# Kernel optimization log

Measured on AMD Instinct MI355X. Metric: run time of the kernel, lower is better.

## Reference

```python
import jax, jax.numpy as jnp
import numpy as np

# ---- static config (matches init_kwargs) ----
N, E = 8192, 262144
IN_CH, MP_CH, HID, K = 128, 512, 256, 10
EPS, DELTA = 1e-3, 0.311
TV_COEFF, BAL_COEFF = 0.785, 0.514


def setup_inputs() -> dict:
    key = jax.random.key(0)
    ks = jax.random.split(key, 16)

    def p(k, shape):
        fan_in = shape[0] if len(shape) > 1 else shape[0]
        return (jax.random.normal(k, shape, jnp.float32) / np.sqrt(fan_in)).astype(jnp.float32)

    return {
        "x": jax.random.normal(ks[0], (N, IN_CH), jnp.float32),
        "edge_index": jax.random.randint(ks[1], (2, E), 0, N, jnp.int32),
        "edge_weight": jax.random.uniform(ks[2], (E,), jnp.float32),
        # GTVConv layer 1 / 2 (Linear weight + bias)
        "W1": p(ks[3], (IN_CH, MP_CH)), "b1": jnp.zeros((MP_CH,), jnp.float32),
        "W2": p(ks[4], (MP_CH, MP_CH)), "b2": jnp.zeros((MP_CH,), jnp.float32),
        # pooling MLP [512 -> 256 -> K], relu, no norm
        "Wm1": p(ks[5], (MP_CH, HID)), "bm1": jnp.zeros((HID,), jnp.float32),
        "Wm2": p(ks[6], (HID, K)), "bm2": jnp.zeros((K,), jnp.float32),
    }


def _gtv_conv(x, src, dst, w, W, b):
    """GTVConv: out = elu( h - delta*(D_G h - Gamma h) + b ),
    gamma_ij = w_ij / max(||h_i - h_j||_1, eps), h = x @ W."""
    h = x @ W                                   # [N, C]
    diff = jnp.sum(jnp.abs(h[src] - h[dst]), axis=-1)   # [E]
    gamma = w / jnp.maximum(diff, EPS)                  # [E]
    deg = jnp.zeros(h.shape[0], h.dtype).at[dst].add(gamma)          # [N]
    agg = jnp.zeros_like(h).at[dst].add(gamma[:, None] * h[src])     # Gamma @ h
    out = h - DELTA * (deg[:, None] * h - agg) + b
    return jax.nn.elu(out)


def reference(x, edge_index, edge_weight, W1, b1, W2, b2, Wm1, bm1, Wm2, bm2):
    src, dst = edge_index[0], edge_index[1]

    h = _gtv_conv(x, src, dst, edge_weight, W1, b1)
    h = _gtv_conv(h, src, dst, edge_weight, W2, b2)

    # pooling MLP -> cluster logits s
    s_logits = jax.nn.relu(h @ Wm1 + bm1) @ Wm2 + bm2   # [N, K]

    # dense adjacency (to_dense_adj: duplicate edges accumulate)
    adj = jnp.zeros((N, N), x.dtype).at[src, dst].add(edge_weight)

    s = jax.nn.softmax(s_logits, axis=-1)

    # total-variation loss: sum_ij a_ij * sum_k |s_ik - s_jk| / (2 * nnz(adj))
    tv = jnp.zeros((), x.dtype)
    for k in range(K):  # small fixed loop over clusters, avoids [N,N,K] tensor
        col = s[:, k]
        tv = tv + jnp.sum(adj * jnp.abs(col[:, None] - col[None, :]))
    n_edges = jax.lax.stop_gradient(jnp.count_nonzero(adj).astype(x.dtype))
    tv = tv / (2.0 * n_edges)

    # asymmetric-norm balance loss (AsymCheegerCut)
    idx = N // K + 1                         # rho-quantile index (static)
    quant = jnp.sort(s, axis=0)[N - idx]     # idx-th largest per cluster, [K]
    t = s - quant[None, :]
    asym = jnp.where(t >= 0, (K - 1) * t, -t)
    denom = float(N * (K - 1))
    bal = (denom - jnp.sum(asym)) / denom

    return s_logits, TV_COEFF * tv, BAL_COEFF * bal
```

## Files before the change

kernel.cpp:

```cpp
#include <hip/hip_runtime.h>

#define N_NODES 8192
#define N_EDGES 262144
#define IN_CH 128
#define MP_CH 512
#define HID 256
#define KCL 10
#define EPS_C 0.001f
#define DELTA_C 0.311f
#define TV_COEFF_C 0.785f
#define BAL_COEFF_C 0.514f
#define RANK1 7373

typedef __bf16 bf16x8 __attribute__((ext_vector_type(8)));
typedef float f32x4 __attribute__((ext_vector_type(4)));
typedef unsigned short ushort8 __attribute__((ext_vector_type(8)));

__device__ __forceinline__ float bf2f(unsigned short h) {
  union { unsigned int u; float f; } c; c.u = ((unsigned int)h) << 16; return c.f;
}
__device__ __forceinline__ unsigned short f2bf(float f) {
  union { float f; unsigned int u; } c; c.f = f;
  unsigned int r = c.u + 0x7fffu + ((c.u >> 16) & 1u);
  return (unsigned short)(r >> 16);
}

__global__ void prep_kernel(const float* __restrict__ x, const float* __restrict__ W1,
                            const float* __restrict__ W2, const float* __restrict__ Wm1,
                            unsigned short* __restrict__ xb, unsigned short* __restrict__ W1bt,
                            unsigned short* __restrict__ W2bt, unsigned short* __restrict__ Wm1bt,
                            const int* __restrict__ dst, int* __restrict__ cnt) {
  int i = blockIdx.x * 256 + threadIdx.x;
  if (i < 1048576) { xb[i] = f2bf(x[i]); return; }
  i -= 1048576;
  if (i < 65536) { int n = i >> 7, k = i & 127; W1bt[i] = f2bf(W1[k * MP_CH + n]); return; }
  i -= 65536;
  if (i < 262144) { int n = i >> 9, k = i & 511; W2bt[i] = f2bf(W2[k * MP_CH + n]); return; }
  i -= 262144;
  if (i < 131072) { int n = i >> 9, k = i & 511; Wm1bt[i] = f2bf(Wm1[k * HID + n]); return; }
  i -= 131072;
  if (i < N_EDGES) atomicAdd(&cnt[dst[i]], 1);
}

__global__ __launch_bounds__(1024) void scan_kernel(const int* __restrict__ cnt,
                                                    int* __restrict__ offs,
                                                    int* __restrict__ cursor) {
  __shared__ int ts[1024];
  int t = threadIdx.x;
  int v[8]; int s = 0;
#pragma unroll
  for (int j = 0; j < 8; ++j) { v[j] = cnt[t * 8 + j]; s += v[j]; }
  ts[t] = s; __syncthreads();
  for (int off = 1; off < 1024; off <<= 1) {
    int add = (t >= off) ? ts[t - off] : 0;
    __syncthreads();
    ts[t] += add;
    __syncthreads();
  }
  int base = ts[t] - s;
#pragma unroll
  for (int j = 0; j < 8; ++j) { offs[t * 8 + j] = base; cursor[t * 8 + j] = base; base += v[j]; }
  if (t == 1023) offs[N_NODES] = ts[1023];
}

__global__ void fill_kernel(const int* __restrict__ src, const int* __restrict__ dst,
                            const float* __restrict__ ew, int* __restrict__ cursor,
                            int2* __restrict__ esw) {
  for (int e = blockIdx.x * blockDim.x + threadIdx.x; e < N_EDGES; e += gridDim.x * blockDim.x) {
    int p = atomicAdd(&cursor[dst[e]], 1);
    esw[p] = make_int2(src[e], __float_as_int(ew[e]));
  }
}

__global__ __launch_bounds__(256) void gemm_bt(
    const unsigned short* __restrict__ A, const unsigned short* __restrict__ BT,
    float* __restrict__ C, unsigned short* __restrict__ Cb,
    const float* __restrict__ bias, int N, int K, int epi) {
  __shared__ unsigned short lA[128 * 32];
  __shared__ unsigned short lB[128 * 32];
  int lane = threadIdx.x & 63;
  int wv = threadIdx.x >> 6;
  int tm = blockIdx.y * 128, tn = blockIdx.x * 128;
  int wm = (wv >> 1) * 64, wn = (wv & 1) * 64;
  int rA = lane & 15, quad = lane >> 4;
  f32x4 acc[4][4];
#pragma unroll
  for (int i = 0; i < 4; ++i)
#pragma unroll
    for (int j = 0; j < 4; ++j) acc[i][j] = (f32x4){0.f, 0.f, 0.f, 0.f};

  int arow = wv * 32 + (lane >> 2);
  int acol = (lane & 3) * 8;

  for (int k0 = 0; k0 < K; k0 += 32) {
#pragma unroll
    for (int c = 0; c < 2; ++c) {
      const unsigned short* ga = A + (size_t)(tm + arow + c * 16) * K + k0 + acol;
      __builtin_amdgcn_global_load_lds(
          (const __attribute__((address_space(1))) unsigned int*)ga,
          (__attribute__((address_space(3))) unsigned int*)(lA + (wv * 32 + c * 16) * 32),
          16, 0, 0);
      const unsigned short* gb = BT + (size_t)(tn + arow + c * 16) * K + k0 + acol;
      __builtin_amdgcn_global_load_lds(
          (const __attribute__((address_space(1))) unsigned int*)gb,
          (__attribute__((address_space(3))) unsigned int*)(lB + (wv * 32 + c * 16) * 32),
          16, 0, 0);
    }
    __syncthreads();
    bf16x8 af[4], bfr[4];
#pragma unroll
    for (int i = 0; i < 4; ++i)
      af[i] = *(const bf16x8*)(lA + (wm + i * 16 + rA) * 32 + quad * 8);
#pragma unroll
    for (int j = 0; j < 4; ++j)
      bfr[j] = *(const bf16x8*)(lB + (wn + j * 16 + rA) * 32 + quad * 8);
#pragma unroll
    for (int i = 0; i < 4; ++i)
#pragma unroll
      for (int j = 0; j < 4; ++j)
        acc[i][j] = __builtin_amdgcn_mfma_f32_16x16x32_bf16(af[i], bfr[j], acc[i][j], 0, 0, 0);
    __syncthreads();
  }

#pragma unroll
  for (int i = 0; i < 4; ++i)
#pragma unroll
    for (int j = 0; j < 4; ++j)
#pragma unroll
      for (int r = 0; r < 4; ++r) {
        int row = tm + wm + i * 16 + quad * 4 + r;
        int col = tn + wn + j * 16 + rA;
        float v = acc[i][j][r];
        size_t idx = (size_t)row * N + col;
        if (epi == 1) { v += bias[col]; v = fmaxf(v, 0.f); C[idx] = v; }
        else { Cb[idx] = f2bf(v); }
      }
}

__global__ __launch_bounds__(256, 8) void gtv_node(
    const unsigned short* __restrict__ hb, const float* __restrict__ bias,
    const int2* __restrict__ esw, const int* __restrict__ offs,
    unsigned short* __restrict__ outb) {
  int lane = threadIdx.x & 63;
  int wv = threadIdx.x >> 6;
  int d = __builtin_amdgcn_readfirstlane(blockIdx.x * 4 + wv);
  ushort8 hdv = ((const ushort8*)(hb + (size_t)d * MP_CH))[lane];
  float hd[8], acc[8];
#pragma unroll
  for (int j = 0; j < 8; ++j) { hd[j] = bf2f(hdv[j]); acc[j] = 0.f; }
  int e0 = offs[d], e1 = offs[d + 1];
  int i = e0;
  for (; i + 1 < e1; i += 2) {
    int2 ma = esw[i], mb = esw[i + 1];
    float wa = __int_as_float(ma.y), wb = __int_as_float(mb.y);
    ushort8 va = ((const ushort8*)(hb + (size_t)ma.x * MP_CH))[lane];
    ushort8 vb = ((const ushort8*)(hb + (size_t)mb.x * MP_CH))[lane];
    float pa = 0.f, pb = 0.f;
#pragma unroll
    for (int j = 0; j < 8; ++j) {
      pa += fabsf(hd[j] - bf2f(va[j]));
      pb += fabsf(hd[j] - bf2f(vb[j]));
    }
#pragma unroll
    for (int m = 1; m < 64; m <<= 1) { pa += __shfl_xor(pa, m, 64); pb += __shfl_xor(pb, m, 64); }
    float ga = wa * __builtin_amdgcn_rcpf(fmaxf(pa, EPS_C));
    float gb = wb * __builtin_amdgcn_rcpf(fmaxf(pb, EPS_C));
#pragma unroll
    for (int j = 0; j < 8; ++j)
      acc[j] += ga * (hd[j] - bf2f(va[j])) + gb * (hd[j] - bf2f(vb[j]));
  }
  if (i < e1) {
    int2 m0 = esw[i];
    float w = __int_as_float(m0.y);
    ushort8 sv = ((const ushort8*)(hb + (size_t)m0.x * MP_CH))[lane];
    float part = 0.f;
#pragma unroll
    for (int j = 0; j < 8; ++j) part += fabsf(hd[j] - bf2f(sv[j]));
#pragma unroll
    for (int m = 1; m < 64; m <<= 1) part += __shfl_xor(part, m, 64);
    float g = w * __builtin_amdgcn_rcpf(fmaxf(part, EPS_C));
#pragma unroll
    for (int j = 0; j < 8; ++j) acc[j] += g * (hd[j] - bf2f(sv[j]));
  }
  const f32x4* br = (const f32x4*)(bias + lane * 8);
  f32x4 b0 = br[0], b1 = br[1];
  unsigned short ov[8];
#pragma unroll
  for (int j = 0; j < 8; ++j) {
    float bv = (j < 4) ? b0[j] : b1[j - 4];
    float o = hd[j] - DELTA_C * acc[j] + bv;
    o = (o > 0.f) ? o : (expf(o) - 1.f);
    ov[j] = f2bf(o);
  }
  *((ushort8*)(outb + (size_t)d * MP_CH) + lane) = *(ushort8*)ov;
}

__global__ __launch_bounds__(256) void gemm_small(
    const float* __restrict__ hm, const float* __restrict__ W,
    const float* __restrict__ b, float* __restrict__ out, float* __restrict__ s) {
  __shared__ float lw[HID * KCL];
  __shared__ float lb[KCL];
  for (int i = threadIdx.x; i < HID * KCL; i += 256) lw[i] = W[i];
  if (threadIdx.x < KCL) lb[threadIdx.x] = b[threadIdx.x];
  __syncthreads();
  int lane = threadIdx.x & 63, wv = threadIdx.x >> 6;
  int row = blockIdx.x * 4 + wv;
  f32x4 hv = *(const f32x4*)(hm + (size_t)row * HID + lane * 4);
  float p[KCL];
#pragma unroll
  for (int n = 0; n < KCL; ++n) {
    int k0 = lane * 4;
    p[n] = hv[0] * lw[(k0 + 0) * KCL + n] + hv[1] * lw[(k0 + 1) * KCL + n] +
           hv[2] * lw[(k0 + 2) * KCL + n] + hv[3] * lw[(k0 + 3) * KCL + n];
  }
#pragma unroll
  for (int n = 0; n < KCL; ++n)
#pragma unroll
    for (int m = 1; m < 64; m <<= 1) p[n] += __shfl_xor(p[n], m, 64);
  if (lane == 0) {
    float vv[KCL]; float mx = -1e30f;
#pragma unroll
    for (int n = 0; n < KCL; ++n) {
      vv[n] = p[n] + lb[n];
      out[(size_t)row * KCL + n] = vv[n];
      mx = fmaxf(mx, vv[n]);
    }
    float sum = 0.f;
#pragma unroll
    for (int n = 0; n < KCL; ++n) { vv[n] = expf(vv[n] - mx); sum += vv[n]; }
    float inv = 1.f / sum;
#pragma unroll
    for (int n = 0; n < KCL; ++n) s[(size_t)row * KCL + n] = vv[n] * inv;
  }
}

__global__ __launch_bounds__(256) void tv_kernel(
    const int* __restrict__ src, const int* __restrict__ dst,
    const float* __restrict__ ew, const float* __restrict__ s,
    unsigned int* __restrict__ bitmap, float* __restrict__ tv_sum) {
  float local = 0.f;
  for (int e = blockIdx.x * blockDim.x + threadIdx.x; e < N_EDGES; e += gridDim.x * blockDim.x) {
    int a = src[e], b = dst[e];
    float w = ew[e];
    const float* sa = s + (size_t)a * KCL;
    const float* sb = s + (size_t)b * KCL;
    float t = 0.f;
#pragma unroll
    for (int k = 0; k < KCL; ++k) t += fabsf(sa[k] - sb[k]);
    local += w * t;
    if (w != 0.f) {
      unsigned int key = ((unsigned int)a << 13) | (unsigned int)b;
      atomicOr(&bitmap[key >> 5], 1u << (key & 31u));
    }
  }
#pragma unroll
  for (int m = 1; m < 64; m <<= 1) local += __shfl_xor(local, m, 64);
  __shared__ float wsum[4];
  int lane = threadIdx.x & 63, wv = threadIdx.x >> 6;
  if (lane == 0) wsum[wv] = local;
  __syncthreads();
  if (threadIdx.x == 0) atomicAdd(tv_sum, wsum[0] + wsum[1] + wsum[2] + wsum[3]);
}

__global__ __launch_bounds__(256) void popc_kernel(const unsigned int* __restrict__ bm,
                                                   int* __restrict__ cnt) {
  int local = 0;
  for (int i = blockIdx.x * blockDim.x + threadIdx.x; i < (1 << 21); i += gridDim.x * blockDim.x)
    local += __popc(bm[i]);
#pragma unroll
  for (int m = 1; m < 64; m <<= 1) local += __shfl_xor(local, m, 64);
  __shared__ int wsum[4];
  int lane = threadIdx.x & 63, wv = threadIdx.x >> 6;
  if (lane == 0) wsum[wv] = local;
  __syncthreads();
  if (threadIdx.x == 0) atomicAdd(cnt, wsum[0] + wsum[1] + wsum[2] + wsum[3]);
}

__global__ __launch_bounds__(1024) void quant_kernel(const float* __restrict__ s,
                                                     float* __restrict__ asym_sum) {
  __shared__ int wcnt[2][16];
  __shared__ float fsum[16];
  int k = blockIdx.x, t = threadIdx.x;
  int lane = t & 63, wv = t >> 6;
  unsigned int v[8];
#pragma unroll
  for (int j = 0; j < 8; ++j)
    v[j] = __float_as_uint(s[(size_t)(t + j * 1024) * KCL + k]);
  unsigned int lo = 0u, hi = 0x3F800000u;
  int p = 0;
  while (lo < hi) {
    unsigned int mid = (lo + hi) >> 1;
    int c = 0;
#pragma unroll
    for (int j = 0; j < 8; ++j) c += (v[j] <= mid) ? 1 : 0;
#pragma unroll
    for (int m = 1; m < 64; m <<= 1) c += __shfl_xor(c, m, 64);
    if (lane == 0) wcnt[p][wv] = c;
    __syncthreads();
    int tot = 0;
#pragma unroll
    for (int i2 = 0; i2 < 16; ++i2) tot += wcnt[p][i2];
    if (tot >= RANK1) hi = mid; else lo = mid + 1;
    p ^= 1;
  }
  float q = __uint_as_float(lo);
  float local = 0.f;
#pragma unroll
  for (int j = 0; j < 8; ++j) {
    float tt = __uint_as_float(v[j]) - q;
    local += (tt >= 0.f) ? 9.f * tt : -tt;
  }
#pragma unroll
  for (int m = 1; m < 64; m <<= 1) local += __shfl_xor(local, m, 64);
  if (lane == 0) fsum[wv] = local;
  __syncthreads();
  if (t == 0) {
    float tot = 0.f;
#pragma unroll
    for (int i2 = 0; i2 < 16; ++i2) tot += fsum[i2];
    atomicAdd(asym_sum, tot);
  }
}

__global__ void finalize_kernel(const float* __restrict__ scal, const int* __restrict__ ne,
                                float* __restrict__ out) {
  if (threadIdx.x == 0) {
    float tv = scal[0], asym = scal[1];
    float nedges = (float)(*ne);
    out[N_NODES * KCL] = TV_COEFF_C * (tv / (2.f * nedges));
    out[N_NODES * KCL + 1] = BAL_COEFF_C * ((73728.f - asym) / 73728.f);
  }
}

#define OFF_BM     ((size_t)0)
#define OFF_HB     ((size_t)16777216)
#define OFF_OUTB   ((size_t)25165824)
#define OFF_HM     ((size_t)33554432)
#define OFF_XB     ((size_t)41943040)
#define OFF_W1BT   ((size_t)44040192)
#define OFF_W2BT   ((size_t)44171264)
#define OFF_WM1BT  ((size_t)44695552)
#define OFF_S      ((size_t)44957696)
#define OFF_CNT    ((size_t)45285376)
#define OFF_OFFS   ((size_t)45318144)
#define OFF_CURSOR ((size_t)45351168)
#define OFF_SCAL   ((size_t)46432512)

extern "C" void kernel_launch(void* const* d_in, const int* in_sizes, int n_in,
                              void* d_out, int out_size, void* d_ws, size_t ws_size,
                              hipStream_t stream) {
  const float* x   = (const float*)d_in[0];
  const int*   ei  = (const int*)d_in[1];
  const float* ew  = (const float*)d_in[2];
  const float* W1  = (const float*)d_in[3];
  const float* b1  = (const float*)d_in[4];
  const float* W2  = (const float*)d_in[5];
  const float* b2  = (const float*)d_in[6];
  const float* Wm1 = (const float*)d_in[7];
  const float* bm1 = (const float*)d_in[8];
  const float* Wm2 = (const float*)d_in[9];
  const float* bm2 = (const float*)d_in[10];
  float* out = (float*)d_out;

  char* ws = (char*)d_ws;
  unsigned int*   bitmap = (unsigned int*)(ws + OFF_BM);
  unsigned short* hb     = (unsigned short*)(ws + OFF_HB);
  unsigned short* outb   = (unsigned short*)(ws + OFF_OUTB);
  float*          hm     = (float*)(ws + OFF_HM);
  int2*           esw    = (int2*)(ws + OFF_HM);
  unsigned short* xb     = (unsigned short*)(ws + OFF_XB);
  unsigned short* W1bt   = (unsigned short*)(ws + OFF_W1BT);
  unsigned short* W2bt   = (unsigned short*)(ws + OFF_W2BT);
  unsigned short* Wm1bt  = (unsigned short*)(ws + OFF_WM1BT);
  float*          s      = (float*)(ws + OFF_S);
  int*            cnt    = (int*)(ws + OFF_CNT);
  int*            offs   = (int*)(ws + OFF_OFFS);
  int*            cursor = (int*)(ws + OFF_CURSOR);
  float*          scal   = (float*)(ws + OFF_SCAL);
  int*            nep    = (int*)(scal + 2);

  const int* srcA = ei;
  const int* dstA = ei + N_EDGES;

  hipMemsetAsync(cnt, 0, N_NODES * sizeof(int), stream);
  hipMemsetAsync(scal, 0, 64, stream);
  hipMemsetAsync(bitmap, 0, (size_t)1 << 23, stream);

  prep_kernel<<<6912, 256, 0, stream>>>(x, W1, W2, Wm1, xb, W1bt, W2bt, Wm1bt, dstA, cnt);
  scan_kernel<<<1, 1024, 0, stream>>>(cnt, offs, cursor);
  fill_kernel<<<1024, 256, 0, stream>>>(srcA, dstA, ew, cursor, esw);

  gemm_bt<<<dim3(MP_CH / 128, N_NODES / 128), 256, 0, stream>>>(
      xb, W1bt, nullptr, hb, nullptr, MP_CH, IN_CH, 2);
  gtv_node<<<N_NODES / 4, 256, 0, stream>>>(hb, b1, esw, offs, outb);
  gemm_bt<<<dim3(MP_CH / 128, N_NODES / 128), 256, 0, stream>>>(
      outb, W2bt, nullptr, hb, nullptr, MP_CH, MP_CH, 2);
  gtv_node<<<N_NODES / 4, 256, 0, stream>>>(hb, b2, esw, offs, outb);
  gemm_bt<<<dim3(HID / 128, N_NODES / 128), 256, 0, stream>>>(
      outb, Wm1bt, hm, nullptr, bm1, HID, MP_CH, 1);
  gemm_small<<<N_NODES / 4, 256, 0, stream>>>(hm, Wm2, bm2, out, s);

  tv_kernel<<<1024, 256, 0, stream>>>(srcA, dstA, ew, s, bitmap, scal);
  popc_kernel<<<1024, 256, 0, stream>>>(bitmap, nep);
  quant_kernel<<<KCL, 1024, 0, stream>>>(s, scal + 1);
  finalize_kernel<<<1, 64, 0, stream>>>(scal, nep, out);
}
```

Measured before the change: 304.3 us.

## Fuse tail kernels, coalesce bf16 GEMM epilogue via LDS, merge memsets

The bf16 GEMM epilogue now stages each 16-row band of accumulators through shared memory and writes 16 contiguous bf16 values per thread, replacing scattered 2-byte stores. The TV-loss and quantile kernels are merged into one launch by splitting blocks between the two roles. Popcount and finalize are merged using a last-block atomic counter. The workspace is rearranged so three memsets become one contiguous memset. Together these cut launch count and uncoalesced stores, at the cost of extra block syncs in the epilogue and a threadfence-based completion check.

```diff
diff --git a/kernel.cpp b/kernel.cpp
--- a/kernel.cpp
+++ b/kernel.cpp
@@ -76,8 +76,9 @@
     const unsigned short* __restrict__ A, const unsigned short* __restrict__ BT,
     float* __restrict__ C, unsigned short* __restrict__ Cb,
     const float* __restrict__ bias, int N, int K, int epi) {
-  __shared__ unsigned short lA[128 * 32];
-  __shared__ unsigned short lB[128 * 32];
+  __shared__ unsigned short lsm[2 * 128 * 32];
+  unsigned short* lA = lsm;
+  unsigned short* lB = lsm + 128 * 32;
   int lane = threadIdx.x & 63;
   int wv = threadIdx.x >> 6;
   int tm = blockIdx.y * 128, tn = blockIdx.x * 128;
@@ -122,19 +123,42 @@
     __syncthreads();
   }
 
-#pragma unroll
-  for (int i = 0; i < 4; ++i)
-#pragma unroll
-    for (int j = 0; j < 4; ++j)
-#pragma unroll
-      for (int r = 0; r < 4; ++r) {
-        int row = tm + wm + i * 16 + quad * 4 + r;
-        int col = tn + wn + j * 16 + rA;
-        float v = acc[i][j][r];
-        size_t idx = (size_t)row * N + col;
-        if (epi == 1) { v += bias[col]; v = fmaxf(v, 0.f); C[idx] = v; }
-        else { Cb[idx] = f2bf(v); }
-      }
+  if (epi == 1) {
+#pragma unroll
+    for (int i = 0; i < 4; ++i)
+#pragma unroll
+      for (int j = 0; j < 4; ++j)
+#pragma unroll
+        for (int r = 0; r < 4; ++r) {
+          int row = tm + wm + i * 16 + quad * 4 + r;
+          int col = tn + wn + j * 16 + rA;
+          float v = acc[i][j][r] + bias[col];
+          C[(size_t)row * N + col] = fmaxf(v, 0.f);
+        }
+  } else {
+    float* fbuf = (float*)lsm;
+    int band = threadIdx.x >> 7;
+    int rrow = (threadIdx.x >> 3) & 15;
+    int cg = threadIdx.x & 7;
+#pragma unroll
+    for (int i = 0; i < 4; ++i) {
+#pragma unroll
+      for (int j = 0; j < 4; ++j)
+#pragma unroll
+        for (int r = 0; r < 4; ++r)
+          fbuf[(wv >> 1) * (16 * 128) + (quad * 4 + r) * 128 + (wn + j * 16 + rA)] =
+              acc[i][j][r];
+      __syncthreads();
+      const float* sr = fbuf + band * (16 * 128) + rrow * 128 + cg * 16;
+      unsigned short ov[16];
+#pragma unroll
+      for (int c = 0; c < 16; ++c) ov[c] = f2bf(sr[c]);
+      size_t base = (size_t)(tm + band * 64 + i * 16 + rrow) * N + tn + cg * 16;
+      *(ushort8*)(Cb + base) = *(ushort8*)ov;
+      *(ushort8*)(Cb + base + 8) = *(ushort8*)(ov + 8);
+      __syncthreads();
+    }
+  }
 }
 
 __global__ __launch_bounds__(256, 8) void gtv_node(
@@ -234,105 +258,117 @@
   }
 }
 
-__global__ __launch_bounds__(256) void tv_kernel(
+__global__ __launch_bounds__(1024) void tvquant_kernel(
     const int* __restrict__ src, const int* __restrict__ dst,
     const float* __restrict__ ew, const float* __restrict__ s,
-    unsigned int* __restrict__ bitmap, float* __restrict__ tv_sum) {
-  float local = 0.f;
-  for (int e = blockIdx.x * blockDim.x + threadIdx.x; e < N_EDGES; e += gridDim.x * blockDim.x) {
-    int a = src[e], b = dst[e];
-    float w = ew[e];
-    const float* sa = s + (size_t)a * KCL;
-    const float* sb = s + (size_t)b * KCL;
-    float t = 0.f;
-#pragma unroll
-    for (int k = 0; k < KCL; ++k) t += fabsf(sa[k] - sb[k]);
-    local += w * t;
-    if (w != 0.f) {
-      unsigned int key = ((unsigned int)a << 13) | (unsigned int)b;
-      atomicOr(&bitmap[key >> 5], 1u << (key & 31u));
-    }
-  }
+    unsigned int* __restrict__ bitmap, float* __restrict__ scal) {
+  __shared__ float fsh[16];
+  __shared__ int wcnt[2][16];
+  int t = threadIdx.x;
+  int lane = t & 63, wv = t >> 6;
+  if (blockIdx.x < 246) {
+    float local = 0.f;
+    for (int e = blockIdx.x * 1024 + t; e < N_EDGES; e += 246 * 1024) {
+      int a = src[e], b = dst[e];
+      float w = ew[e];
+      const float* sa = s + (size_t)a * KCL;
+      const float* sb = s + (size_t)b * KCL;
+      float tv = 0.f;
+#pragma unroll
+      for (int k = 0; k < KCL; ++k) tv += fabsf(sa[k] - sb[k]);
+      local += w * tv;
+      if (w != 0.f) {
+        unsigned int key = ((unsigned int)a << 13) | (unsigned int)b;
+        atomicOr(&bitmap[key >> 5], 1u << (key & 31u));
+      }
+    }
+#pragma unroll
+    for (int m = 1; m < 64; m <<= 1) local += __shfl_xor(local, m, 64);
+    if (lane == 0) fsh[wv] = local;
+    __syncthreads();
+    if (t == 0) {
+      float tot = 0.f;
+#pragma unroll
+      for (int i2 = 0; i2 < 16; ++i2) tot += fsh[i2];
+      atomicAdd(&scal[0], tot);
+    }
+  } else {
+    int k = blockIdx.x - 246;
+    unsigned int v[8];
+#pragma unroll
+    for (int j = 0; j < 8; ++j)
+      v[j] = __float_as_uint(s[(size_t)(t + j * 1024) * KCL + k]);
+    unsigned int lo = 0u, hi = 0x3F800000u;
+    int p = 0;
+    while (lo < hi) {
+      unsigned int mid = (lo + hi) >> 1;
+      int c = 0;
+#pragma unroll
+      for (int j = 0; j < 8; ++j) c += (v[j] <= mid) ? 1 : 0;
+#pragma unroll
+      for (int m = 1; m < 64; m <<= 1) c += __shfl_xor(c, m, 64);
+      if (lane == 0) wcnt[p][wv] = c;
+      __syncthreads();
+      int tot = 0;
+#pragma unroll
+      for (int i2 = 0; i2 < 16; ++i2) tot += wcnt[p][i2];
+      if (tot >= RANK1) hi = mid; else lo = mid + 1;
+      p ^= 1;
+    }
+    float q = __uint_as_float(lo);
+    float local = 0.f;
+#pragma unroll
+    for (int j = 0; j < 8; ++j) {
+      float tt = __uint_as_float(v[j]) - q;
+      local += (tt >= 0.f) ? 9.f * tt : -tt;
+    }
+#pragma unroll
+    for (int m = 1; m < 64; m <<= 1) local += __shfl_xor(local, m, 64);
+    if (lane == 0) fsh[wv] = local;
+    __syncthreads();
+    if (t == 0) {
+      float tot = 0.f;
+#pragma unroll
+      for (int i2 = 0; i2 < 16; ++i2) tot += fsh[i2];
+      atomicAdd(&scal[1], tot);
+    }
+  }
+}
+
+__global__ __launch_bounds__(1024) void popcfin_kernel(const unsigned int* __restrict__ bm,
+                                                       float* __restrict__ scal,
+                                                       float* __restrict__ out) {
+  __shared__ int ish[16];
+  int t = threadIdx.x;
+  int lane = t & 63, wv = t >> 6;
+  int local = 0;
+  for (int i = blockIdx.x * 1024 + t; i < (1 << 21); i += 256 * 1024)
+    local += __popc(bm[i]);
 #pragma unroll
   for (int m = 1; m < 64; m <<= 1) local += __shfl_xor(local, m, 64);
-  __shared__ float wsum[4];
-  int lane = threadIdx.x & 63, wv = threadIdx.x >> 6;
-  if (lane == 0) wsum[wv] = local;
-  __syncthreads();
-  if (threadIdx.x == 0) atomicAdd(tv_sum, wsum[0] + wsum[1] + wsum[2] + wsum[3]);
-}
-
-__global__ __launch_bounds__(256) void popc_kernel(const unsigned int* __restrict__ bm,
-                                                   int* __restrict__ cnt) {
-  int local = 0;
-  for (int i = blockIdx.x * blockDim.x + threadIdx.x; i < (1 << 21); i += gridDim.x * blockDim.x)
-    local += __popc(bm[i]);
-#pragma unroll
-  for (int m = 1; m < 64; m <<= 1) local += __shfl_xor(local, m, 64);
-  __shared__ int wsum[4];
-  int lane = threadIdx.x & 63, wv = threadIdx.x >> 6;
-  if (lane == 0) wsum[wv] = local;
-  __syncthreads();
-  if (threadIdx.x == 0) atomicAdd(cnt, wsum[0] + wsum[1] + wsum[2] + wsum[3]);
-}
-
-__global__ __launch_bounds__(1024) void quant_kernel(const float* __restrict__ s,
-                                                     float* __restrict__ asym_sum) {
-  __shared__ int wcnt[2][16];
-  __shared__ float fsum[16];
-  int k = blockIdx.x, t = threadIdx.x;
-  int lane = t & 63, wv = t >> 6;
-  unsigned int v[8];
-#pragma unroll
-  for (int j = 0; j < 8; ++j)
-    v[j] = __float_as_uint(s[(size_t)(t + j * 1024) * KCL + k]);
-  unsigned int lo = 0u, hi = 0x3F800000u;
-  int p = 0;
-  while (lo < hi) {
-    unsigned int mid = (lo + hi) >> 1;
-    int c = 0;
-#pragma unroll
-    for (int j = 0; j < 8; ++j) c += (v[j] <= mid) ? 1 : 0;
-#pragma unroll
-    for (int m = 1; m < 64; m <<= 1) c += __shfl_xor(c, m, 64);
-    if (lane == 0) wcnt[p][wv] = c;
-    __syncthreads();
-    int tot = 0;
-#pragma unroll
-    for (int i2 = 0; i2 < 16; ++i2) tot += wcnt[p][i2];
-    if (tot >= RANK1) hi = mid; else lo = mid + 1;
-    p ^= 1;
-  }
-  float q = __uint_as_float(lo);
-  float local = 0.f;
-#pragma unroll
-  for (int j = 0; j < 8; ++j) {
-    float tt = __uint_as_float(v[j]) - q;
-    local += (tt >= 0.f) ? 9.f * tt : -tt;
-  }
-#pragma unroll
-  for (int m = 1; m < 64; m <<= 1) local += __shfl_xor(local, m, 64);
-  if (lane == 0) fsum[wv] = local;
+  if (lane == 0) ish[wv] = local;
   __syncthreads();
   if (t == 0) {
-    float tot = 0.f;
-#pragma unroll
-    for (int i2 = 0; i2 < 16; ++i2) tot += fsum[i2];
-    atomicAdd(asym_sum, tot);
-  }
-}
-
-__global__ void finalize_kernel(const float* __restrict__ scal, const int* __restrict__ ne,
-                                float* __restrict__ out) {
-  if (threadIdx.x == 0) {
-    float tv = scal[0], asym = scal[1];
-    float nedges = (float)(*ne);
-    out[N_NODES * KCL] = TV_COEFF_C * (tv / (2.f * nedges));
-    out[N_NODES * KCL + 1] = BAL_COEFF_C * ((73728.f - asym) / 73728.f);
+    int tot = 0;
+#pragma unroll
+    for (int i2 = 0; i2 < 16; ++i2) tot += ish[i2];
+    atomicAdd((int*)(scal + 2), tot);
+    __threadfence();
+    int d = atomicAdd((int*)(scal + 3), 1);
+    if (d == 255) {
+      float tv = scal[0], asym = scal[1];
+      float nedges = (float)(*(int*)(scal + 2));
+      out[N_NODES * KCL] = TV_COEFF_C * (tv / (2.f * nedges));
+      out[N_NODES * KCL + 1] = BAL_COEFF_C * ((73728.f - asym) / 73728.f);
+    }
   }
 }
 
 #define OFF_BM     ((size_t)0)
+#define OFF_CNT    ((size_t)8388608)
+#define OFF_SCAL   ((size_t)8421376)
+#define OFF_OFFS   ((size_t)8421888)
+#define OFF_CURSOR ((size_t)8454912)
 #define OFF_HB     ((size_t)16777216)
 #define OFF_OUTB   ((size_t)25165824)
 #define OFF_HM     ((size_t)33554432)
@@ -341,10 +377,6 @@
 #define OFF_W2BT   ((size_t)44171264)
 #define OFF_WM1BT  ((size_t)44695552)
 #define OFF_S      ((size_t)44957696)
-#define OFF_CNT    ((size_t)45285376)
-#define OFF_OFFS   ((size_t)45318144)
-#define OFF_CURSOR ((size_t)45351168)
-#define OFF_SCAL   ((size_t)46432512)
 
 extern "C" void kernel_launch(void* const* d_in, const int* in_sizes, int n_in,
                               void* d_out, int out_size, void* d_ws, size_t ws_size,
@@ -364,6 +396,10 @@
 
   char* ws = (char*)d_ws;
   unsigned int*   bitmap = (unsigned int*)(ws + OFF_BM);
+  int*            cnt    = (int*)(ws + OFF_CNT);
+  float*          scal   = (float*)(ws + OFF_SCAL);
+  int*            offs   = (int*)(ws + OFF_OFFS);
+  int*            cursor = (int*)(ws + OFF_CURSOR);
   unsigned short* hb     = (unsigned short*)(ws + OFF_HB);
   unsigned short* outb   = (unsigned short*)(ws + OFF_OUTB);
   float*          hm     = (float*)(ws + OFF_HM);
@@ -373,18 +409,11 @@
   unsigned short* W2bt   = (unsigned short*)(ws + OFF_W2BT);
   unsigned short* Wm1bt  = (unsigned short*)(ws + OFF_WM1BT);
   float*          s      = (float*)(ws + OFF_S);
-  int*            cnt    = (int*)(ws + OFF_CNT);
-  int*            offs   = (int*)(ws + OFF_OFFS);
-  int*            cursor = (int*)(ws + OFF_CURSOR);
-  float*          scal   = (float*)(ws + OFF_SCAL);
-  int*            nep    = (int*)(scal + 2);
 
   const int* srcA = ei;
   const int* dstA = ei + N_EDGES;
 
-  hipMemsetAsync(cnt, 0, N_NODES * sizeof(int), stream);
-  hipMemsetAsync(scal, 0, 64, stream);
-  hipMemsetAsync(bitmap, 0, (size_t)1 << 23, stream);
+  hipMemsetAsync(ws, 0, 8421632, stream);
 
   prep_kernel<<<6912, 256, 0, stream>>>(x, W1, W2, Wm1, xb, W1bt, W2bt, Wm1bt, dstA, cnt);
   scan_kernel<<<1, 1024, 0, stream>>>(cnt, offs, cursor);
@@ -400,8 +429,6 @@
       outb, Wm1bt, hm, nullptr, bm1, HID, MP_CH, 1);
   gemm_small<<<N_NODES / 4, 256, 0, stream>>>(hm, Wm2, bm2, out, s);
 
-  tv_kernel<<<1024, 256, 0, stream>>>(srcA, dstA, ew, s, bitmap, scal);
-  popc_kernel<<<1024, 256, 0, stream>>>(bitmap, nep);
-  quant_kernel<<<KCL, 1024, 0, stream>>>(s, scal + 1);
-  finalize_kernel<<<1, 64, 0, stream>>>(scal, nep, out);
-}
+  tvquant_kernel<<<256, 1024, 0, stream>>>(srcA, dstA, ew, s, bitmap, scal);
+  popcfin_kernel<<<256, 1024, 0, stream>>>(bitmap, scal, out);
+}
```

Result: faster. 261.5 us (-14.1%).
